# Kernel tuning notes

Hardware: AMD Instinct MI355X
Metric: run time of the kernel (lower is better)

Reference implementation:

```python
import jax, jax.numpy as jnp
import numpy as np

K = 5  # kernel_size (odd -> 'same' output size given the pad in semi_conv)
B, C_IN, C_OUT, H, W = 4, 8, 16, 192, 192
NEG_INF = -jnp.inf  # aggregation identity of the (max, +) semifield


def setup_inputs() -> dict:
    key = jax.random.key(0)
    kx, ks = jax.random.split(key)
    x = jax.random.normal(kx, (B, C_IN, H, W), dtype=jnp.float32)
    # torch.rand((C_out, C_in)) -> uniform(0,1); lower-bounded at 0.25 to avoid
    # numerically extreme kernels from near-zero scales (division by 4*scale).
    scales = jax.random.uniform(ks, (C_OUT, C_IN), dtype=jnp.float32, minval=0.25, maxval=1.0)
    return {"x": x, "scales": scales}


def _compute_kernel(scales):
    # matches torch.linspace(-K//2 + 1, K//2, K) with Python floor division
    start = (-K) // 2 + 1
    z_i = jnp.linspace(float(start), float(K // 2), K, dtype=jnp.float32)
    z = z_i[:, None] ** 2 + z_i[None, :] ** 2                  # [K, K]
    return -z[None, None, :, :] / (4.0 * scales[:, :, None, None])  # [C_out, C_in, K, K]


def _maxplus_conv(x, w):
    # result[b,co,h,w] = sum_ci max_{i,j} ( x_pad[b,ci,h+i,w+j] + w[co,ci,i,j] )
    b, c_in, h, wd = x.shape
    c_out = w.shape[0]
    p = K // 2
    xp = jnp.pad(x, ((0, 0), (0, 0), (p, p), (p, p)), constant_values=NEG_INF)
    # running max over the K*K kernel offsets; avoids the [B,Co,Ci,K*K,H*W] unfold blow-up
    acc = jnp.full((b, c_out, c_in, h, wd), NEG_INF, dtype=x.dtype)
    for i in range(K):
        for j in range(K):
            patch = xp[:, None, :, i:i + h, j:j + wd]           # [B,1,C_in,H,W]
            wij = w[None, :, :, i, j][..., None, None]          # [1,C_out,C_in,1,1]
            acc = jnp.maximum(acc, patch + wij)
    return jnp.sum(acc, axis=2)                                 # [B,C_out,H,W]


def reference(x, scales):
    return _maxplus_conv(x, _compute_kernel(scales))
```

## Files before the change

kernel.cpp:

```cpp
#include <hip/hip_runtime.h>
#include <cmath>

#define B_    4
#define CIN   8
#define COUT  16
#define H_    192
#define W_    192
#define TW    32
#define TH    16
#define SX    36
#define SY    20
#define NCO   4
#define NT    256
#define SLAB  (SY * SX)
#define NF2   (SLAB / 2)
#define CHAN_F2 (H_ * W_ / 2)

__global__ __launch_bounds__(NT, 4)
void semiconv_kernel(const float* __restrict__ x,
                     const float* __restrict__ scales,
                     float* __restrict__ out) {
    __shared__ float tile[CIN * SLAB];
    __shared__ float wtab[NCO * CIN];

    int blk = blockIdx.x;
    const int tile_x = blk % 6;  blk /= 6;
    const int tile_y = blk % 12; blk /= 12;
    const int cg     = blk & 3;  blk >>= 2;
    const int b      = blk;

    const int tid = threadIdx.x;
    const int lt  = tid & 127;
    const int grp = tid >> 7;
    const int py  = lt >> 3;
    const int p0  = (lt & 7) * 4;

    if (tid < NCO * CIN)
        wtab[tid] = 0.25f / scales[cg * NCO * CIN + tid];

    const int gy0  = tile_y * TH - 2;
    const int gxp0 = tile_x * (TW / 2) - 1;
    int gidx[2]; bool okk[2];
    {
        int e = tid;
        #pragma unroll
        for (int k = 0; k < 2; ++k) {
            int ey = e / 18, ex = e - ey * 18;
            int gy = gy0 + ey, gxp = gxp0 + ex;
            okk[k]  = (gy >= 0) && (gy < H_) && (gxp >= 0) && (gxp < W_ / 2);
            gidx[k] = gy * (W_ / 2) + gxp;
            e += NT;
        }
    }
    const bool tail = tid < (NF2 - NT);

    const float2* xb = (const float2*)(x + (size_t)b * CIN * H_ * W_);
    const float2 NEG2 = make_float2(-INFINITY, -INFINITY);
    float2 pf[CIN][2];
    #pragma unroll
    for (int ci = 0; ci < CIN; ++ci) {
        const float2* xp = xb + ci * CHAN_F2;
        pf[ci][0] = okk[0] ? xp[gidx[0]] : NEG2;
        pf[ci][1] = (tail && okk[1]) ? xp[gidx[1]] : NEG2;
    }
    float2* lp = (float2*)tile;
    #pragma unroll
    for (int ci = 0; ci < CIN; ++ci) {
        lp[ci * NF2 + tid] = pf[ci][0];
        if (tail) lp[ci * NF2 + tid + NT] = pf[ci][1];
    }

    __syncthreads();

    float wa[NCO][4];
    #pragma unroll
    for (int c = 0; c < NCO; ++c)
        #pragma unroll
        for (int k = 0; k < 4; ++k)
            wa[c][k] = wtab[c * CIN + grp * 4 + k];

    float acc[NCO][4];
    #pragma unroll
    for (int c = 0; c < NCO; ++c)
        #pragma unroll
        for (int p = 0; p < 4; ++p) acc[c][p] = 0.f;

    const float* tb = tile + grp * 4 * SLAB + py * SX + p0;

    #pragma unroll
    for (int k = 0; k < 4; ++k) {
        const float* tp = tb + k * SLAB;

        float X[5][8];
        #pragma unroll
        for (int r = 0; r < 5; ++r) {
            float4 lo = *(const float4*)(tp + r * SX);
            float4 hi = *(const float4*)(tp + r * SX + 4);
            X[r][0] = lo.x; X[r][1] = lo.y; X[r][2] = lo.z; X[r][3] = lo.w;
            X[r][4] = hi.x; X[r][5] = hi.y; X[r][6] = hi.z; X[r][7] = hi.w;
        }

        float V0[8], V1[8], V4[8];
        #pragma unroll
        for (int c = 0; c < 8; ++c) {
            V0[c] = X[2][c];
            V1[c] = fmaxf(X[1][c], X[3][c]);
            V4[c] = fmaxf(X[0][c], X[4][c]);
        }

        float A1[NCO], A2[NCO], A4[NCO], A5[NCO], A8[NCO];
        #pragma unroll
        for (int c = 0; c < NCO; ++c) {
            float a = wa[c][k];
            A1[c] = a;
            A2[c] = a + a;
            A4[c] = A2[c] + A2[c];
            A5[c] = A4[c] + a;
            A8[c] = A4[c] + A4[c];
        }

        #pragma unroll
        for (int p = 0; p < 4; ++p) {
            const int c = p + 2;
            float M0 = V0[c];
            float M1 = fmaxf(fmaxf(V0[c - 1], V0[c + 1]), V1[c]);
            float M2 = fmaxf(V1[c - 1], V1[c + 1]);
            float M4 = fmaxf(fmaxf(V0[c - 2], V0[c + 2]), V4[c]);
            float M5 = fmaxf(fmaxf(V1[c - 2], V1[c + 2]),
                             fmaxf(V4[c - 1], V4[c + 1]));
            float M8 = fmaxf(V4[c - 2], V4[c + 2]);
            #pragma unroll
            for (int co = 0; co < NCO; ++co) {
                float lo3 = fmaxf(fmaxf(M1 - A1[co], M2 - A2[co]), M0);
                float hi3 = fmaxf(fmaxf(M4 - A4[co], M5 - A5[co]),
                                  M8 - A8[co]);
                acc[co][p] += fmaxf(lo3, hi3);
            }
        }
    }

    float* cbuf = tile + 4 * SLAB;
    if (grp == 1) {
        float4* cb = (float4*)(cbuf + lt * 16);
        #pragma unroll
        for (int co = 0; co < NCO; ++co)
            cb[co] = make_float4(acc[co][0], acc[co][1], acc[co][2], acc[co][3]);
    }
    __syncthreads();
    if (grp == 0) {
        const float4* cb = (const float4*)(cbuf + lt * 16);
        const int gy = tile_y * TH + py;
        const int gx = tile_x * TW + p0;
        #pragma unroll
        for (int co = 0; co < NCO; ++co) {
            float4 o = cb[co];
            float* op = out + ((size_t)((b * COUT + cg * NCO + co) * H_) + gy) * W_ + gx;
            *(float4*)op = make_float4(acc[co][0] + o.x, acc[co][1] + o.y,
                                       acc[co][2] + o.z, acc[co][3] + o.w);
        }
    }
}

extern "C" void kernel_launch(void* const* d_in, const int* in_sizes, int n_in,
                              void* d_out, int out_size, void* d_ws, size_t ws_size,
                              hipStream_t stream) {
    const float* x      = (const float*)d_in[0];
    const float* scales = (const float*)d_in[1];
    float* out          = (float*)d_out;

    const int n_blocks = B_ * (COUT / NCO) * (H_ / TH) * (W_ / TW);
    semiconv_kernel<<<n_blocks, NT, 0, stream>>>(x, scales, out);
}
```

Baseline: 16.95 us.

## Double output channels per block, split input channels four ways, use packed float2 math

Each block now computes 8 output channels with 512 threads, and four thread groups each handle 2 input channels. This halves the number of blocks, so each input tile is staged into shared memory half as many times. The partial sums from the four groups are reduced through a separate shared buffer before one group writes the result. The weight subtractions and accumulations use 2-wide vector types, intended to map to packed FP32 instructions. In exchange the launch has fewer blocks, the reduction stage is larger, and register and LDS pressure per block rise.

```diff
diff --git a/kernel.cpp b/kernel.cpp
--- a/kernel.cpp
+++ b/kernel.cpp
@@ -1,5 +1,7 @@
 #include <hip/hip_runtime.h>
 #include <cmath>
+
+typedef float v2f __attribute__((ext_vector_type(2)));
 
 #define B_    4
 #define CIN   8
@@ -10,23 +12,24 @@
 #define TH    16
 #define SX    36
 #define SY    20
-#define NCO   4
-#define NT    256
 #define SLAB  (SY * SX)
 #define NF2   (SLAB / 2)
+#define NCO   8
+#define NT    512
 #define CHAN_F2 (H_ * W_ / 2)
 
 __global__ __launch_bounds__(NT, 4)
 void semiconv_kernel(const float* __restrict__ x,
                      const float* __restrict__ scales,
                      float* __restrict__ out) {
-    __shared__ float tile[CIN * SLAB];
-    __shared__ float wtab[NCO * CIN];
+    __shared__ __align__(16) float tile[CIN * SLAB];
+    __shared__ __align__(16) float wtab[CIN][NCO];
+    __shared__ __align__(16) float cbuf[3 * NCO * 128 * 4];
 
     int blk = blockIdx.x;
     const int tile_x = blk % 6;  blk /= 6;
     const int tile_y = blk % 12; blk /= 12;
-    const int cg     = blk & 3;  blk >>= 2;
+    const int cg     = blk & 1;  blk >>= 1;
     const int b      = blk;
 
     const int tid = threadIdx.x;
@@ -35,61 +38,43 @@
     const int py  = lt >> 3;
     const int p0  = (lt & 7) * 4;
 
-    if (tid < NCO * CIN)
-        wtab[tid] = 0.25f / scales[cg * NCO * CIN + tid];
+    if (tid < CIN * NCO) {
+        int ci = tid >> 3, co = tid & 7;
+        wtab[ci][co] = 0.25f / scales[(cg * NCO + co) * CIN + ci];
+    }
 
-    const int gy0  = tile_y * TH - 2;
-    const int gxp0 = tile_x * (TW / 2) - 1;
-    int gidx[2]; bool okk[2];
-    {
-        int e = tid;
+    if (tid < NF2) {
+        const int ey  = tid / 18, ex = tid - (tid / 18) * 18;
+        const int gy  = tile_y * TH - 2 + ey;
+        const int gxp = tile_x * (TW / 2) - 1 + ex;
+        const bool ok = (gy >= 0) && (gy < H_) && (gxp >= 0) && (gxp < W_ / 2);
+        const int gofs = gy * (W_ / 2) + gxp;
+        const float2* xb = (const float2*)(x + (size_t)b * CIN * H_ * W_);
+        const float2 NEG2 = make_float2(-INFINITY, -INFINITY);
+        float2 v[CIN];
         #pragma unroll
-        for (int k = 0; k < 2; ++k) {
-            int ey = e / 18, ex = e - ey * 18;
-            int gy = gy0 + ey, gxp = gxp0 + ex;
-            okk[k]  = (gy >= 0) && (gy < H_) && (gxp >= 0) && (gxp < W_ / 2);
-            gidx[k] = gy * (W_ / 2) + gxp;
-            e += NT;
-        }
-    }
-    const bool tail = tid < (NF2 - NT);
-
-    const float2* xb = (const float2*)(x + (size_t)b * CIN * H_ * W_);
-    const float2 NEG2 = make_float2(-INFINITY, -INFINITY);
-    float2 pf[CIN][2];
-    #pragma unroll
-    for (int ci = 0; ci < CIN; ++ci) {
-        const float2* xp = xb + ci * CHAN_F2;
-        pf[ci][0] = okk[0] ? xp[gidx[0]] : NEG2;
-        pf[ci][1] = (tail && okk[1]) ? xp[gidx[1]] : NEG2;
-    }
-    float2* lp = (float2*)tile;
-    #pragma unroll
-    for (int ci = 0; ci < CIN; ++ci) {
-        lp[ci * NF2 + tid] = pf[ci][0];
-        if (tail) lp[ci * NF2 + tid + NT] = pf[ci][1];
+        for (int ci = 0; ci < CIN; ++ci)
+            v[ci] = ok ? xb[ci * CHAN_F2 + gofs] : NEG2;
+        float2* lp = (float2*)tile;
+        #pragma unroll
+        for (int ci = 0; ci < CIN; ++ci)
+            lp[ci * NF2 + tid] = v[ci];
     }
 
     __syncthreads();
 
-    float wa[NCO][4];
+    v2f acc[NCO][2];
     #pragma unroll
-    for (int c = 0; c < NCO; ++c)
-        #pragma unroll
-        for (int k = 0; k < 4; ++k)
-            wa[c][k] = wtab[c * CIN + grp * 4 + k];
+    for (int co = 0; co < NCO; ++co) {
+        acc[co][0] = (v2f){0.f, 0.f};
+        acc[co][1] = (v2f){0.f, 0.f};
+    }
 
-    float acc[NCO][4];
-    #pragma unroll
-    for (int c = 0; c < NCO; ++c)
-        #pragma unroll
-        for (int p = 0; p < 4; ++p) acc[c][p] = 0.f;
-
-    const float* tb = tile + grp * 4 * SLAB + py * SX + p0;
+    const float* tbg = tile + grp * 2 * SLAB + py * SX + p0;
 
     #pragma unroll
-    for (int k = 0; k < 4; ++k) {
-        const float* tp = tb + k * SLAB;
+    for (int k = 0; k < 2; ++k) {
+        const float* tp = tbg + k * SLAB;
 
         float X[5][8];
         #pragma unroll
@@ -108,55 +93,76 @@
             V4[c] = fmaxf(X[0][c], X[4][c]);
         }
 
-        float A1[NCO], A2[NCO], A4[NCO], A5[NCO], A8[NCO];
+        v2f M0[2], M1[2], M2[2], M4[2], M5[2], M8[2];
         #pragma unroll
-        for (int c = 0; c < NCO; ++c) {
-            float a = wa[c][k];
-            A1[c] = a;
-            A2[c] = a + a;
-            A4[c] = A2[c] + A2[c];
-            A5[c] = A4[c] + a;
-            A8[c] = A4[c] + A4[c];
+        for (int pr = 0; pr < 2; ++pr) {
+            const int c0 = 2 + 2 * pr;
+            M0[pr] = (v2f){V0[c0], V0[c0 + 1]};
+            M1[pr] = (v2f){fmaxf(fmaxf(V0[c0 - 1], V0[c0 + 1]), V1[c0]),
+                           fmaxf(fmaxf(V0[c0],     V0[c0 + 2]), V1[c0 + 1])};
+            M2[pr] = (v2f){fmaxf(V1[c0 - 1], V1[c0 + 1]),
+                           fmaxf(V1[c0],     V1[c0 + 2])};
+            M4[pr] = (v2f){fmaxf(fmaxf(V0[c0 - 2], V0[c0 + 2]), V4[c0]),
+                           fmaxf(fmaxf(V0[c0 - 1], V0[c0 + 3]), V4[c0 + 1])};
+            M5[pr] = (v2f){fmaxf(fmaxf(fmaxf(V1[c0 - 2], V1[c0 + 2]), V4[c0 - 1]), V4[c0 + 1]),
+                           fmaxf(fmaxf(fmaxf(V1[c0 - 1], V1[c0 + 3]), V4[c0]),     V4[c0 + 2])};
+            M8[pr] = (v2f){fmaxf(V4[c0 - 2], V4[c0 + 2]),
+                           fmaxf(V4[c0 - 1], V4[c0 + 3])};
         }
 
+        const float* wrow = &wtab[grp * 2 + k][0];
+        float4 wv0 = *(const float4*)(wrow);
+        float4 wv1 = *(const float4*)(wrow + 4);
+
         #pragma unroll
-        for (int p = 0; p < 4; ++p) {
-            const int c = p + 2;
-            float M0 = V0[c];
-            float M1 = fmaxf(fmaxf(V0[c - 1], V0[c + 1]), V1[c]);
-            float M2 = fmaxf(V1[c - 1], V1[c + 1]);
-            float M4 = fmaxf(fmaxf(V0[c - 2], V0[c + 2]), V4[c]);
-            float M5 = fmaxf(fmaxf(V1[c - 2], V1[c + 2]),
-                             fmaxf(V4[c - 1], V4[c + 1]));
-            float M8 = fmaxf(V4[c - 2], V4[c + 2]);
+        for (int co = 0; co < NCO; ++co) {
+            const float a = (co < 4) ? (&wv0.x)[co] : (&wv1.x)[co - 4];
+            const v2f aa = (v2f){a, a};
             #pragma unroll
-            for (int co = 0; co < NCO; ++co) {
-                float lo3 = fmaxf(fmaxf(M1 - A1[co], M2 - A2[co]), M0);
-                float hi3 = fmaxf(fmaxf(M4 - A4[co], M5 - A5[co]),
-                                  M8 - A8[co]);
-                acc[co][p] += fmaxf(lo3, hi3);
+            for (int pr = 0; pr < 2; ++pr) {
+                v2f s1 = M1[pr] - aa;
+                v2f s2 = M2[pr] - 2.f * aa;
+                v2f s4 = M4[pr] - 4.f * aa;
+                v2f s5 = M5[pr] - 5.f * aa;
+                v2f s8 = M8[pr] - 8.f * aa;
+                float lox = fmaxf(fmaxf(s1.x, s2.x), M0[pr].x);
+                float hix = fmaxf(fmaxf(s4.x, s5.x), s8.x);
+                float loy = fmaxf(fmaxf(s1.y, s2.y), M0[pr].y);
+                float hiy = fmaxf(fmaxf(s4.y, s5.y), s8.y);
+                v2f vm;
+                vm.x = fmaxf(lox, hix);
+                vm.y = fmaxf(loy, hiy);
+                acc[co][pr] += vm;
             }
         }
     }
 
-    float* cbuf = tile + 4 * SLAB;
-    if (grp == 1) {
-        float4* cb = (float4*)(cbuf + lt * 16);
+    if (grp != 0) {
+        float* cb = cbuf + (((grp - 1) * NCO) * 128 + lt) * 4;
         #pragma unroll
-        for (int co = 0; co < NCO; ++co)
-            cb[co] = make_float4(acc[co][0], acc[co][1], acc[co][2], acc[co][3]);
+        for (int co = 0; co < NCO; ++co) {
+            float* p = cb + co * 128 * 4;
+            *(v2f*)p       = acc[co][0];
+            *(v2f*)(p + 2) = acc[co][1];
+        }
     }
     __syncthreads();
     if (grp == 0) {
-        const float4* cb = (const float4*)(cbuf + lt * 16);
         const int gy = tile_y * TH + py;
         const int gx = tile_x * TW + p0;
         #pragma unroll
         for (int co = 0; co < NCO; ++co) {
-            float4 o = cb[co];
+            #pragma unroll
+            for (int g = 1; g < 4; ++g) {
+                float4 t = *(const float4*)(cbuf + (((g - 1) * NCO + co) * 128 + lt) * 4);
+                acc[co][0] += (v2f){t.x, t.y};
+                acc[co][1] += (v2f){t.z, t.w};
+            }
+            float4 o;
+            o.x = acc[co][0].x; o.y = acc[co][0].y;
+            o.z = acc[co][1].x; o.w = acc[co][1].y;
             float* op = out + ((size_t)((b * COUT + cg * NCO + co) * H_) + gy) * W_ + gx;
-            *(float4*)op = make_float4(acc[co][0] + o.x, acc[co][1] + o.y,
-                                       acc[co][2] + o.z, acc[co][3] + o.w);
+            *(float4*)op = o;
         }
     }
 }
@@ -168,6 +174,6 @@
     const float* scales = (const float*)d_in[1];
     float* out          = (float*)d_out;
 
-    const int n_blocks = B_ * (COUT / NCO) * (H_ / TH) * (W_ / TW);
+    const int n_blocks = B_ * 2 * (H_ / TH) * (W_ / TW);
     semiconv_kernel<<<n_blocks, NT, 0, stream>>>(x, scales, out);
 }
```

After: 16.05 us (median of 2 runs). 1.06x faster.
